# Kernel optimization log

Hardware: AMD Instinct MI355X
Metric: run time of the kernel (lower is better)

## Reference

```python
import jax, jax.numpy as jnp
import numpy as np

NUM_HEADS = 16
H_SELF = 10  # hardcoded h in forward: first 10 heads self-attend, rest cross-attend
DIM = 1024
HEAD_DIM = DIM // NUM_HEADS
SCALE = HEAD_DIM ** -0.5


def _qkv(x, Wqkv):
    # x: [B, N, C] -> q, k, v each [B, H, N, hd]
    B, N, C = x.shape
    qkv = (x @ Wqkv).reshape(B, N, 3, NUM_HEADS, C // NUM_HEADS).transpose(2, 0, 3, 1, 4)
    return qkv[0], qkv[1], qkv[2]


def _attn(q, k, v):
    # q,k,v: [B, h, N, d]
    scores = jnp.einsum('bhqd,bhkd->bhqk', q, k) * SCALE
    probs = jax.nn.softmax(scores, axis=-1)  # attn_drop_ratio = 0.0
    return jnp.einsum('bhqk,bhkd->bhqd', probs, v)


def _proj(xa, xb, Wproj, bproj):
    # xa: [B, 10, N, d], xb: [B, 6, N, d] -> [B, N, C]
    B = xa.shape[0]
    N = xa.shape[2]
    x = jnp.concatenate([xa, xb], axis=1).transpose(0, 2, 1, 3).reshape(B, N, DIM)
    return x @ Wproj + bproj  # proj_drop_ratio = 0.0


def setup_inputs() -> dict:
    key = jax.random.key(0)
    k0, k1, k2, k3 = jax.random.split(key, 4)
    B, N, C = 16, 577, DIM
    x1 = jax.random.normal(k0, (B, N, C), dtype=jnp.float32)
    x2 = jax.random.normal(k1, (B, N, C), dtype=jnp.float32)
    # nn.Linear(dim, dim*3, bias=False): store as [C, 3C] so y = x @ W
    Wqkv = jax.random.normal(k2, (C, 3 * C), dtype=jnp.float32) * 0.02
    # nn.Linear(dim, dim) has bias by default
    Wproj = jax.random.normal(k3, (C, C), dtype=jnp.float32) * 0.02
    bproj = jnp.zeros((C,), dtype=jnp.float32)
    return {"x1": x1, "x2": x2, "Wqkv": Wqkv, "Wproj": Wproj, "bproj": bproj}


def reference(x1, x2, Wqkv, Wproj, bproj):
    q1, k1, v1 = _qkv(x1, Wqkv)
    q2, k2, v2 = _qkv(x2, Wqkv)
    h = H_SELF
    x11 = _attn(q1[:, :h], k1[:, :h], v1[:, :h])  # self-attn branch of x1
    x12 = _attn(q1[:, h:], k2[:, h:], v2[:, h:])  # cross: q from x1, kv from x2
    x22 = _attn(q2[:, :h], k2[:, :h], v2[:, :h])  # self-attn branch of x2
    x21 = _attn(q2[:, h:], k1[:, h:], v1[:, h:])  # cross: q from x2, kv from x1
    out1 = _proj(x11, x12, Wproj, bproj)
    out2 = _proj(x22, x21, Wproj, bproj)
    return (out1, out2)
```

## Files before the change

kernel.cpp:

```cpp
#include <hip/hip_runtime.h>
#include <hip/hip_bf16.h>
#include <stdint.h>
#include <math.h>

typedef __attribute__((ext_vector_type(8))) short bf16x8;
typedef __attribute__((ext_vector_type(4))) float f32x4;
typedef __attribute__((ext_vector_type(8))) unsigned short ushort8;
typedef __attribute__((ext_vector_type(4))) unsigned int uint4v;
typedef __attribute__((ext_vector_type(2))) unsigned int uint2v;

#define NTOK   9232
#define MROWS  18464
#define MPAD   18688
#define NPADV  640
#define QSCALE 0.18033688011112042f

__device__ __forceinline__ uint16_t f2b(float f) {
  uint32_t u = __builtin_bit_cast(uint32_t, f);
  u += 0x7fffu + ((u >> 16) & 1u);
  return (uint16_t)(u >> 16);
}

__device__ __forceinline__ uint32_t packbf(float lo, float hi) {
  return (uint32_t)f2b(lo) | ((uint32_t)f2b(hi) << 16);
}

__device__ __forceinline__ f32x4 mfma16(bf16x8 a, bf16x8 b, f32x4 c) {
  return __builtin_amdgcn_mfma_f32_16x16x32_bf16(a, b, c, 0, 0, 0);
}

__device__ __forceinline__ void gl_lds16(const void* g, void* l) {
  __builtin_amdgcn_global_load_lds(
      (const __attribute__((address_space(1))) uint32_t*)g,
      (__attribute__((address_space(3))) uint32_t*)l, 16, 0, 0);
}

__global__ void convert_x_kernel(const float* __restrict__ x1,
                                 const float* __restrict__ x2,
                                 uint16_t* __restrict__ Xb) {
  const size_t stride = (size_t)gridDim.x * blockDim.x;
  const size_t total8 = (size_t)MPAD * 1024 / 8;
  for (size_t i = (size_t)blockIdx.x * blockDim.x + threadIdx.x; i < total8; i += stride) {
    const size_t e = i * 8;
    const size_t row = e >> 10;
    ushort8 ov;
    if (row < (size_t)MROWS) {
      const float* src = (row < (size_t)NTOK) ? (x1 + e) : (x2 + (e - (size_t)NTOK * 1024));
      float4 a = *(const float4*)(src);
      float4 b = *(const float4*)(src + 4);
      ov[0] = f2b(a.x); ov[1] = f2b(a.y); ov[2] = f2b(a.z); ov[3] = f2b(a.w);
      ov[4] = f2b(b.x); ov[5] = f2b(b.y); ov[6] = f2b(b.z); ov[7] = f2b(b.w);
    } else {
      ov = (ushort8)0;
    }
    *(ushort8*)(Xb + e) = ov;
  }
}

__global__ void transw_kernel(const float* __restrict__ in, uint16_t* __restrict__ out,
                              int R, int Cc) {
  __shared__ float t[32][33];
  const int r0 = blockIdx.x * 32, c0 = blockIdx.y * 32;
  const int tr = threadIdx.x >> 5, tc = threadIdx.x & 31;
#pragma unroll
  for (int i = 0; i < 4; ++i)
    t[tr + i * 8][tc] = in[(size_t)(r0 + tr + i * 8) * Cc + c0 + tc];
  __syncthreads();
#pragma unroll
  for (int i = 0; i < 4; ++i) {
    const int orow = c0 + tr + i * 8;
    out[(size_t)orow * R + r0 + tc] = f2b(t[tc][tr + i * 8]);
  }
}

__global__ void zero_vpad_kernel(uint16_t* __restrict__ Vtb) {
  const int idx = blockIdx.x * 256 + threadIdx.x;
  for (int i = idx; i < 32768 * 8; i += 256 * 256) {
    const int p = i >> 3;
    const int ch = i & 7;
    *(ushort8*)(Vtb + (size_t)p * NPADV + 576 + ch * 8) = (ushort8)0;
  }
}

#define G256_SETUP                                                             \
  const int srow = tt >> 2;                                        \
  const int schunk = tt & 3;                         \
  const int swc = schunk ^ ((srow >> 1) & 3);                                  \
  const int crs = (c >> 1) & 3;                                                \
  char* aL = (char*)As3;                                                       \
  char* bL = (char*)Bs3;                                                       \
  auto SA = [&](int buf, int t) {                                              \
    _Pragma("unroll")                                                          \
    for (int i = 0; i < 2; ++i) {                                              \
      const int row = i * 128 + srow;                                          \
      gl_lds16(aG + (size_t)row * 2048 + t * 64 + (swc << 4),                  \
               aL + buf * 16384 + row * 64 + (schunk << 4));                   \
    }                                                                          \
  };                                                                           \
  auto SB = [&](int buf, int t) {                                              \
    _Pragma("unroll")                                                          \
    for (int i = 0; i < 2; ++i) {                                              \
      const int row = i * 128 + srow;                                          \
      gl_lds16(bG + (size_t)row * 2048 + t * 64 + (swc << 4),                  \
               bL + buf * 16384 + row * 64 + (schunk << 4));                   \
    }                                                                          \
  };                                                                           \
  auto LDA = [&](int buf, int mi) -> bf16x8 {                                  \
    const int r = wm * 128 + mi * 16 + c;                                      \
    return *(const bf16x8*)(aL + buf * 16384 + r * 64 + ((g ^ crs) << 4));     \
  };                                                                           \
  auto LDB = [&](int buf, int ni) -> bf16x8 {                                  \
    const int r = wn * 64 + ni * 16 + c;                                       \
    return *(const bf16x8*)(bL + buf * 16384 + r * 64 + ((g ^ crs) << 4));     \
  };

#define G256_MFMA_BLOCK(BR)                                                    \
  {                                                                            \
    bf16x8 b0 = LDB(BR, 0), b1 = LDB(BR, 1);                                   \
    bf16x8 b2 = LDB(BR, 2), b3 = LDB(BR, 3);                                   \
    __builtin_amdgcn_s_setprio(1);                                             \
    _Pragma("unroll")                                                          \
    for (int mi = 0; mi < 8; ++mi) {                                           \
      const bf16x8 a0 = LDA(BR, mi);                                           \
      acc[mi][0] = mfma16(a0, b0, acc[mi][0]);                                 \
      acc[mi][1] = mfma16(a0, b1, acc[mi][1]);                                 \
      acc[mi][2] = mfma16(a0, b2, acc[mi][2]);                                 \
      acc[mi][3] = mfma16(a0, b3, acc[mi][3]);                                 \
    }                                                                          \
    __builtin_amdgcn_s_setprio(0);                                             \
  }

#define G256R2_ITER(T, BR)                                                     \
  {                                                                            \
    asm volatile("s_waitcnt vmcnt(0)" ::: "memory");                           \
    __builtin_amdgcn_s_barrier();                                              \
    __builtin_amdgcn_sched_barrier(0);                                         \
    if ((T) < 31) { SA((BR) ^ 1, (T) + 1); SB((BR) ^ 1, (T) + 1); }            \
    G256_MFMA_BLOCK(BR)                                                        \
  }

#define G256_KLOOP                                                             \
  G256_SETUP                                                                   \
  SA(0, 0); SB(0, 0);                                                          \
  for (int j2 = 0; j2 < 16; ++j2) {                                            \
    G256R2_ITER(2 * j2, 0)                                                     \
    G256R2_ITER(2 * j2 + 1, 1)                                                 \
  }

__global__ __launch_bounds__(512, 1) void gemm_qkv_kernel(
    const uint16_t* __restrict__ A, const uint16_t* __restrict__ Bt,
    uint16_t* __restrict__ Qb, uint16_t* __restrict__ Kb, uint16_t* __restrict__ Vtb) {
  __shared__ __align__(128) char smem[65536];
  uint16_t* As3 = (uint16_t*)smem;
  uint16_t* Bs3 = (uint16_t*)(smem + 32768);
  const int tt = threadIdx.x;
  const int w = tt >> 6, l = tt & 63;
  const int c = l & 15, g = l >> 4;
  const int wm = w >> 2, wn = w & 3;
  const int orig = blockIdx.x;
  const int xcd = orig & 7, sub8 = orig >> 3;
  const int work = (xcd < 4 ? xcd * 110 : 440 + (xcd - 4) * 109) + sub8;
  int bm, bn;
  {
    const int stripe = work / 36;
    if (stripe >= 24) { bm = 72; bn = work - 864; }
    else {
      const int r2 = work % 36;
      const int bg = r2 / 12, r3 = r2 % 12;
      bm = stripe * 3 + r3 % 3;
      bn = bg * 4 + r3 / 3;
    }
  }
  f32x4 acc[8][4] = {};
  const char* aG = (const char*)(A + (size_t)bm * 256 * 1024);
  const char* bG = (const char*)(Bt + (size_t)bn * 256 * 1024);

  G256_KLOOP

  const int sArea = bn >> 2;
  __syncthreads();
  if (sArea <= 1) {
    uint16_t* outb = (sArea == 0) ? Qb : Kb;
    const float scale = (sArea == 0) ? QSCALE : 1.0f;
#pragma unroll
    for (int q = 0; q < 4; ++q) {
      if (wm == (q >> 1)) {
        char* wbase = smem + (g * 4) * 544 + (wn * 64 + c) * 2;
#pragma unroll
        for (int mi2 = 0; mi2 < 4; ++mi2) {
          const int mi = (q & 1) * 4 + mi2;
#pragma unroll
          for (int r = 0; r < 4; ++r)
#pragma unroll
            for (int ni = 0; ni < 4; ++ni)
              *(uint16_t*)(wbase + mi2 * 8704 + r * 544 + ni * 32) =
                  f2b(acc[mi][ni][r] * scale);
        }
      }
      __syncthreads();
      {
        const int row = tt >> 3, hp = tt & 7;
        const int R = bm * 256 + q * 64 + row;
        if (R < MROWS) {
          const int src = (R >= NTOK) ? 1 : 0;
          const int rr = R - src * NTOK;
          const int bb = rr / 577;
          const int nn = rr - bb * 577;
          const size_t base0 =
              ((((size_t)src * 16 + bb) * 16 + (bn & 3) * 4) * 577 + nn) * 64;
          const char* rbase = smem + row * 544;
#pragma unroll
          for (int j = 0; j < 4; ++j) {
            const int ch = hp + j * 8;
            const int hh2 = ch >> 3;
            const int dd = (ch & 7) * 8;
            const uint4v v = *(const uint4v*)(rbase + ch * 16);
            *(uint4v*)(outb + base0 + (size_t)hh2 * 577 * 64 + dd) = v;
          }
        }
      }
      __syncthreads();
    }
  } else {
#pragma unroll
    for (int half = 0; half < 2; ++half) {
#pragma unroll
      for (int hv = 0; hv < 2; ++hv) {
        if (wm == half && (wn >> 1) == hv) {
          char* wbase = smem + ((wn & 1) * 64 + c) * 272 + g * 8;
#pragma unroll
          for (int mi = 0; mi < 8; ++mi)
#pragma unroll
            for (int ni = 0; ni < 4; ++ni) {
              const uint2v pw = {packbf(acc[mi][ni][0], acc[mi][ni][1]),
                                 packbf(acc[mi][ni][2], acc[mi][ni][3])};
              *(uint2v*)(wbase + ni * 4352 + mi * 32) = pw;
            }
        }
        __syncthreads();
        {
          const int col = tt >> 2, s = tt & 3;
          const int C = bn * 256 + hv * 128 + col;
          const int hh2 = (C >> 6) & 15;
          const int dd = C & 63;
          const char* rbase = smem + col * 272 + s * 64;
#pragma unroll
          for (int j = 0; j < 4; ++j) {
            const int R0 = bm * 256 + half * 128 + s * 32 + j * 8;
            if (R0 >= MROWS) continue;
            const int src0 = (R0 >= NTOK) ? 1 : 0;
            const int rr0 = R0 - src0 * NTOK;
            const int bb0 = rr0 / 577;
            const int nn0 = rr0 - bb0 * 577;
            const uint4v v = *(const uint4v*)(rbase + j * 16);
            const uint16_t* pv = (const uint16_t*)&v;
            const bool fast = (R0 + 7 < MROWS) && (nn0 + 8 <= 577) &&
                              (((R0 + 7) >= NTOK ? 1 : 0) == src0);
            if (fast) {
              uint16_t* dst =
                  Vtb + ((((size_t)src0 * 16 + bb0) * 16 + hh2) * 64 + dd) * NPADV + nn0;
#pragma unroll
              for (int e = 0; e < 8; ++e) dst[e] = pv[e];
            } else {
#pragma unroll
              for (int e = 0; e < 8; ++e) {
                const int R = R0 + e;
                if (R >= MROWS) break;
                const int sx = (R >= NTOK) ? 1 : 0;
                const int rr = R - sx * NTOK;
                const int b2 = rr / 577;
                const int n2 = rr - b2 * 577;
                Vtb[((((size_t)sx * 16 + b2) * 16 + hh2) * 64 + dd) * NPADV + n2] = pv[e];
              }
            }
          }
        }
        __syncthreads();
      }
    }
  }
}

#define GEMM_TRI_SETUP                                                         \
  const int srow4 = tt >> 2;                                        \
  const int schunk = tt & 3;                         \
  const int swc = schunk ^ ((srow4 >> 1) & 3);                                 \
  const int crs = (c >> 1) & 3;                                                \
  char* aL = (char*)As3;                                                       \
  char* bL = (char*)Bs3;                                                       \
  auto SA = [&](int buf, int t) {                                              \
    _Pragma("unroll")                                                          \
    for (int i = 0; i < 2; ++i) {                                              \
      const int row = i * 64 + srow4;                                          \
      gl_lds16(aG + (size_t)row * 2048 + t * 64 + (swc << 4),                  \
               aL + buf * 8192 + row * 64 + (schunk << 4));                    \
    }                                                                          \
  };                                                                           \
  auto SB = [&](int buf, int t) {                                              \
    _Pragma("unroll")                                                          \
    for (int i = 0; i < 2; ++i) {                                              \
      const int row = i * 64 + srow4;                                          \
      gl_lds16(bG + (size_t)row * 2048 + t * 64 + (swc << 4),                  \
               bL + buf * 8192 + row * 64 + (schunk << 4));                    \
    }                                                                          \
  };                                                                           \
  auto LDA = [&](int buf, int mi) -> bf16x8 {                                  \
    const int r = wm * 64 + mi * 16 + c;                                       \
    return *(const bf16x8*)(aL + buf * 8192 + r * 64 + ((g ^ crs) << 4));      \
  };                                                                           \
  auto LDB = [&](int buf, int ni) -> bf16x8 {                                  \
    const int r = wn * 64 + ni * 16 + c;                                       \
    return *(const bf16x8*)(bL + buf * 8192 + r * 64 + ((g ^ crs) << 4));      \
  };

#define G_MFMA_BLOCK(BR)                                                       \
  {                                                                            \
    bf16x8 b0 = LDB(BR, 0), b1 = LDB(BR, 1);                                   \
    bf16x8 b2 = LDB(BR, 2), b3 = LDB(BR, 3);                                   \
    __builtin_amdgcn_s_setprio(1);                                             \
    _Pragma("unroll")                                                          \
    for (int mi = 0; mi < 4; ++mi) {                                           \
      const bf16x8 a0 = LDA(BR, mi);                                           \
      acc[mi][0] = mfma16(a0, b0, acc[mi][0]);                                 \
      acc[mi][1] = mfma16(a0, b1, acc[mi][1]);                                 \
      acc[mi][2] = mfma16(a0, b2, acc[mi][2]);                                 \
      acc[mi][3] = mfma16(a0, b3, acc[mi][3]);                                 \
    }                                                                          \
    __builtin_amdgcn_s_setprio(0);                                             \
  }

#define G_ITER_S(T, BR, BS)                                                    \
  {                                                                            \
    asm volatile("s_waitcnt vmcnt(4)" ::: "memory");                           \
    __builtin_amdgcn_s_barrier();                                              \
    __builtin_amdgcn_sched_barrier(0);                                         \
    SA(BS, (T) + 2); SB(BS, (T) + 2);                                          \
    G_MFMA_BLOCK(BR)                                                           \
  }

#define G_ITER_N(BR, VM)                                                       \
  {                                                                            \
    asm volatile("s_waitcnt vmcnt(" #VM ")" ::: "memory");                     \
    __builtin_amdgcn_s_barrier();                                              \
    __builtin_amdgcn_sched_barrier(0);                                         \
    G_MFMA_BLOCK(BR)                                                           \
  }

#define GEMM_TRI_KLOOP                                                         \
  GEMM_TRI_SETUP                                                               \
  SA(0, 0); SB(0, 0); SA(1, 1); SB(1, 1);                                      \
  for (int j = 0; j < 10; ++j) {                                               \
    const int t3 = j * 3;                                                      \
    G_ITER_S(t3, 0, 2)                                                         \
    G_ITER_S(t3 + 1, 1, 0)                                                     \
    G_ITER_S(t3 + 2, 2, 1)                                                     \
  }                                                                            \
  G_ITER_N(0, 4)                                                               \
  G_ITER_N(1, 0)

#define KVB 64
#define ATT_NT 10
__global__ __launch_bounds__(256, 2) void attn_kernel(
    const uint16_t* __restrict__ Qb, const uint16_t* __restrict__ Kb,
    const uint16_t* __restrict__ Vtb, uint16_t* __restrict__ O) {
  __shared__ __align__(128) char smem[73728];
  const int tid = threadIdx.x;
  const int w = tid >> 6, l = tid & 63;
  const int c = l & 15, g = l >> 4;
  const int bid = blockIdx.x;
  const int qc = bid & 1;
  const int p = bid >> 1;
  const int h = p & 15, b = (p >> 4) & 15, o = p >> 8;
  const int kvsrc = (h < 10) ? o : (1 - o);
  const uint16_t* qp = Qb + (((size_t)o * 16 + b) * 16 + h) * 577 * 64;
  const uint16_t* kp = Kb + (((size_t)kvsrc * 16 + b) * 16 + h) * 577 * 64;
  const uint16_t* vp = Vtb + (((size_t)kvsrc * 16 + b) * 16 + h) * 64 * NPADV;

  const int qbase = qc * 320 + w * 80;

  const int sub = l >> 3;
  const int colEl = (((l & 7) ^ sub) << 3);
  char* KsA = smem;
  char* VsA = smem + 16384;
  char* Pb  = smem + 32768 + w * 10240;
  const int rs = (c & 7) << 4;

  bf16x8 Qf[5][2];
#pragma unroll
  for (int qt = 0; qt < 5; ++qt) {
    const int qrow = min(qbase + qt * 16 + c, 576);
    const uint16_t* qr = qp + (size_t)qrow * 64 + g * 8;
    Qf[qt][0] = *(const bf16x8*)(qr);
    Qf[qt][1] = *(const bf16x8*)(qr + 32);
  }

  f32x4 acc[4][5] = {};
  float m_run[5] = {-3.0e38f, -3.0e38f, -3.0e38f, -3.0e38f, -3.0e38f};
  float l_run[5] = {0.f, 0.f, 0.f, 0.f, 0.f};

  auto STAGE = [&](int buf, int kv0) {
#pragma unroll
    for (int i = 0; i < 2; ++i) {
      const int j = w * 2 + i;
      const int row = j * 8 + sub;
      const int gk = min(kv0 + row, 576);
      gl_lds16(kp + (size_t)gk * 64 + colEl, KsA + buf * 8192 + j * 1024 + l * 16);
      gl_lds16(vp + (size_t)row * NPADV + kv0 + colEl, VsA + buf * 8192 + j * 1024 + l * 16);
    }
  };

  STAGE(0, 0);
  __syncthreads();

  for (int t = 0; t < ATT_NT; ++t) {
    if (t < ATT_NT - 1) STAGE((t + 1) & 1, (t + 1) * KVB);
    {
      const char* Kt = KsA + (t & 1) * 8192;
      const char* Vt = VsA + (t & 1) * 8192;
      bf16x8 Kf[4][2];
#pragma unroll
      for (int kt = 0; kt < 4; ++kt) {
        const char* kr = Kt + (kt * 16 + c) * 128;
        Kf[kt][0] = *(const bf16x8*)(kr + ((g * 16) ^ rs));
        Kf[kt][1] = *(const bf16x8*)(kr + ((64 + g * 16) ^ rs));
      }
      float alpha_[5];
#pragma unroll
      for (int qt = 0; qt < 5; ++qt) {
        f32x4 s[4];
#pragma unroll
        for (int kt = 0; kt < 4; ++kt) {
          f32x4 z = {0.f, 0.f, 0.f, 0.f};
          z = mfma16(Kf[kt][0], Qf[qt][0], z);
          z = mfma16(Kf[kt][1], Qf[qt][1], z);
          s[kt] = z;
        }
        if (t == ATT_NT - 1) {
#pragma unroll
          for (int kt = 0; kt < 4; ++kt)
#pragma unroll
            for (int r = 0; r < 4; ++r) {
              if (kt == 0 && r == 0) { if (g > 0) s[kt][r] = -3.0e38f; }
              else s[kt][r] = -3.0e38f;
            }
        }
        float mt = s[0][0];
#pragma unroll
        for (int kt = 0; kt < 4; ++kt)
#pragma unroll
          for (int r = 0; r < 4; ++r) mt = fmaxf(mt, s[kt][r]);
        mt = fmaxf(mt, __shfl_xor(mt, 16));
        mt = fmaxf(mt, __shfl_xor(mt, 32));
        float al;
        if (mt > m_run[qt] + 8.0f) {
          al = exp2f(m_run[qt] - mt);
          m_run[qt] = mt;
        } else {
          al = 1.0f;
        }
        alpha_[qt] = al;
        const float mcur = m_run[qt];
        float lt = 0.f;
#pragma unroll
        for (int kt = 0; kt < 4; ++kt)
#pragma unroll
          for (int r = 0; r < 4; ++r) {
            const float pv = exp2f(s[kt][r] - mcur);
            s[kt][r] = pv;
            lt += pv;
          }
        lt += __shfl_xor(lt, 16);
        lt += __shfl_xor(lt, 32);
        l_run[qt] = l_run[qt] * al + lt;
        const int rowOff = (qt * 16 + c) * 128;
#pragma unroll
        for (int kt = 0; kt < 4; ++kt) {
          const uint2v pw = {packbf(s[kt][0], s[kt][1]), packbf(s[kt][2], s[kt][3])};
          *(uint2v*)(Pb + rowOff + ((kt * 32 + g * 8) ^ rs)) = pw;
        }
      }
#pragma unroll
      for (int qt = 0; qt < 5; ++qt) {
        if (alpha_[qt] != 1.0f) {
#pragma unroll
          for (int dt = 0; dt < 4; ++dt)
#pragma unroll
            for (int r = 0; r < 4; ++r) acc[dt][qt][r] *= alpha_[qt];
        }
      }
      bf16x8 pf[5][2];
#pragma unroll
      for (int qt = 0; qt < 5; ++qt) {
        const char* pr = Pb + (qt * 16 + c) * 128;
        pf[qt][0] = *(const bf16x8*)(pr + ((g * 16) ^ rs));
        pf[qt][1] = *(const bf16x8*)(pr + ((64 + g * 16) ^ rs));
      }
#pragma unroll
      for (int dt = 0; dt < 4; ++dt) {
        const char* vr = Vt + (dt * 16 + c) * 128;
        const bf16x8 v0 = *(const bf16x8*)(vr + ((g * 16) ^ rs));
        const bf16x8 v1 = *(const bf16x8*)(vr + ((64 + g * 16) ^ rs));
#pragma unroll
        for (int qt = 0; qt < 5; ++qt) {
          acc[dt][qt] = mfma16(v0, pf[qt][0], acc[dt][qt]);
          acc[dt][qt] = mfma16(v1, pf[qt][1], acc[dt][qt]);
        }
      }
    }
    __syncthreads();
  }

  {
#pragma unroll
    for (int qt = 0; qt < 5; ++qt) {
      const float inv = 1.0f / l_run[qt];
      const int rowOff = (qt * 16 + c) * 128;
#pragma unroll
      for (int dt = 0; dt < 4; ++dt) {
        const uint2v pw = {packbf(acc[dt][qt][0] * inv, acc[dt][qt][1] * inv),
                           packbf(acc[dt][qt][2] * inv, acc[dt][qt][3] * inv)};
        *(uint2v*)(Pb + rowOff + ((dt * 32 + g * 8) ^ rs)) = pw;
      }
    }
    const size_t obase = ((size_t)o * NTOK + (size_t)b * 577) * 1024 + h * 64;
#pragma unroll
    for (int pass = 0; pass < 10; ++pass) {
      const int row = pass * 8 + (l >> 3);
      const int tok = qbase + row;
      const uint4v vv = *(const uint4v*)(Pb + row * 128 + (((l & 7) * 16) ^ ((row & 7) << 4)));
      if (tok <= 576)
        *(uint4v*)(O + obase + (size_t)tok * 1024 + (l & 7) * 8) = vv;
    }
  }
}

__global__ __launch_bounds__(256, 3) void gemm_proj_kernel(
    const uint16_t* __restrict__ A, const uint16_t* __restrict__ Bt,
    const float* __restrict__ bias, float* __restrict__ out) {
  __shared__ uint16_t As3[3][4096];
  __shared__ uint16_t Bs3[3][4096];
  const int tt = threadIdx.x;
  const int w = tt >> 6, l = tt & 63;
  const int c = l & 15, g = l >> 4;
  const int wgid = blockIdx.x;
  const int work = (wgid & 7) * 145 + (wgid >> 3);
  int bm, bn;
  {
    const int stripe = work / 48;
    if (stripe >= 24) { bm = 144; bn = work - 24 * 48; }
    else { const int r3 = work % 48; bm = stripe * 6 + r3 % 6; bn = r3 / 6; }
  }
  const int wm = w >> 1, wn = w & 1;
  f32x4 acc[4][4] = {};
  const char* aG = (const char*)(A + (size_t)bm * 128 * 1024);
  const char* bG = (const char*)(Bt + (size_t)bn * 128 * 1024);

  GEMM_TRI_KLOOP

#pragma unroll
  for (int mi = 0; mi < 4; ++mi) {
#pragma unroll
    for (int r = 0; r < 4; ++r) {
      const int R = bm * 128 + wm * 64 + mi * 16 + g * 4 + r;
      if (R >= MROWS) continue;
#pragma unroll
      for (int ni = 0; ni < 4; ++ni) {
        const int C = bn * 128 + wn * 64 + ni * 16 + c;
        out[(size_t)R * 1024 + C] = acc[mi][ni][r] + bias[C];
      }
    }
  }
}

extern "C" void kernel_launch(void* const* d_in, const int* in_sizes, int n_in,
                              void* d_out, int out_size, void* d_ws, size_t ws_size,
                              hipStream_t stream) {
  (void)in_sizes; (void)n_in; (void)out_size; (void)ws_size;
  const float* x1    = (const float*)d_in[0];
  const float* x2    = (const float*)d_in[1];
  const float* Wqkv  = (const float*)d_in[2];
  const float* Wproj = (const float*)d_in[3];
  const float* bproj = (const float*)d_in[4];
  float* out = (float*)d_out;

  char* ws = (char*)d_ws;
  size_t off = 0;
  auto alloc = [&](size_t bytes) -> char* {
    char* p = ws + off;
    off += (bytes + 255) & ~(size_t)255;
    return p;
  };
  uint16_t* Xb     = (uint16_t*)alloc((size_t)MPAD * 1024 * 2);
  uint16_t* Wqkvt  = (uint16_t*)alloc((size_t)3072 * 1024 * 2);
  uint16_t* Wprojt = (uint16_t*)alloc((size_t)1024 * 1024 * 2);
  uint16_t* Qb     = (uint16_t*)alloc((size_t)512 * 577 * 64 * 2);
  uint16_t* Kb     = (uint16_t*)alloc((size_t)512 * 577 * 64 * 2);
  uint16_t* Vtb    = (uint16_t*)alloc((size_t)512 * 64 * NPADV * 2);

  zero_vpad_kernel<<<256, 256, 0, stream>>>(Vtb);
  convert_x_kernel<<<2048, 256, 0, stream>>>(x1, x2, Xb);
  transw_kernel<<<dim3(32, 96), 256, 0, stream>>>(Wqkv, Wqkvt, 1024, 3072);
  transw_kernel<<<dim3(32, 32), 256, 0, stream>>>(Wproj, Wprojt, 1024, 1024);
  gemm_qkv_kernel<<<876, 512, 0, stream>>>(Xb, Wqkvt, Qb, Kb, Vtb);
  attn_kernel<<<1024, 256, 0, stream>>>(Qb, Kb, Vtb, Xb );
  gemm_proj_kernel<<<1160, 256, 0, stream>>>(Xb, Wprojt, bproj, out);
}
```

Before: 347.9 us.

## Retile projection GEMM to 256x256 blocks and prioritize attention MFMAs

```diff
diff --git a/kernel.cpp b/kernel.cpp
--- a/kernel.cpp
+++ b/kernel.cpp
@@ -281,82 +281,45 @@
   }
 }
 
-#define GEMM_TRI_SETUP                                                         \
-  const int srow4 = tt >> 2;                                        \
-  const int schunk = tt & 3;                         \
-  const int swc = schunk ^ ((srow4 >> 1) & 3);                                 \
-  const int crs = (c >> 1) & 3;                                                \
-  char* aL = (char*)As3;                                                       \
-  char* bL = (char*)Bs3;                                                       \
-  auto SA = [&](int buf, int t) {                                              \
-    _Pragma("unroll")                                                          \
-    for (int i = 0; i < 2; ++i) {                                              \
-      const int row = i * 64 + srow4;                                          \
-      gl_lds16(aG + (size_t)row * 2048 + t * 64 + (swc << 4),                  \
-               aL + buf * 8192 + row * 64 + (schunk << 4));                    \
-    }                                                                          \
-  };                                                                           \
-  auto SB = [&](int buf, int t) {                                              \
-    _Pragma("unroll")                                                          \
-    for (int i = 0; i < 2; ++i) {                                              \
-      const int row = i * 64 + srow4;                                          \
-      gl_lds16(bG + (size_t)row * 2048 + t * 64 + (swc << 4),                  \
-               bL + buf * 8192 + row * 64 + (schunk << 4));                    \
-    }                                                                          \
-  };                                                                           \
-  auto LDA = [&](int buf, int mi) -> bf16x8 {                                  \
-    const int r = wm * 64 + mi * 16 + c;                                       \
-    return *(const bf16x8*)(aL + buf * 8192 + r * 64 + ((g ^ crs) << 4));      \
-  };                                                                           \
-  auto LDB = [&](int buf, int ni) -> bf16x8 {                                  \
-    const int r = wn * 64 + ni * 16 + c;                                       \
-    return *(const bf16x8*)(bL + buf * 8192 + r * 64 + ((g ^ crs) << 4));      \
-  };
-
-#define G_MFMA_BLOCK(BR)                                                       \
-  {                                                                            \
-    bf16x8 b0 = LDB(BR, 0), b1 = LDB(BR, 1);                                   \
-    bf16x8 b2 = LDB(BR, 2), b3 = LDB(BR, 3);                                   \
-    __builtin_amdgcn_s_setprio(1);                                             \
-    _Pragma("unroll")                                                          \
-    for (int mi = 0; mi < 4; ++mi) {                                           \
-      const bf16x8 a0 = LDA(BR, mi);                                           \
-      acc[mi][0] = mfma16(a0, b0, acc[mi][0]);                                 \
-      acc[mi][1] = mfma16(a0, b1, acc[mi][1]);                                 \
-      acc[mi][2] = mfma16(a0, b2, acc[mi][2]);                                 \
-      acc[mi][3] = mfma16(a0, b3, acc[mi][3]);                                 \
-    }                                                                          \
-    __builtin_amdgcn_s_setprio(0);                                             \
-  }
-
-#define G_ITER_S(T, BR, BS)                                                    \
-  {                                                                            \
-    asm volatile("s_waitcnt vmcnt(4)" ::: "memory");                           \
-    __builtin_amdgcn_s_barrier();                                              \
-    __builtin_amdgcn_sched_barrier(0);                                         \
-    SA(BS, (T) + 2); SB(BS, (T) + 2);                                          \
-    G_MFMA_BLOCK(BR)                                                           \
-  }
-
-#define G_ITER_N(BR, VM)                                                       \
-  {                                                                            \
-    asm volatile("s_waitcnt vmcnt(" #VM ")" ::: "memory");                     \
-    __builtin_amdgcn_s_barrier();                                              \
-    __builtin_amdgcn_sched_barrier(0);                                         \
-    G_MFMA_BLOCK(BR)                                                           \
-  }
-
-#define GEMM_TRI_KLOOP                                                         \
-  GEMM_TRI_SETUP                                                               \
-  SA(0, 0); SB(0, 0); SA(1, 1); SB(1, 1);                                      \
-  for (int j = 0; j < 10; ++j) {                                               \
-    const int t3 = j * 3;                                                      \
-    G_ITER_S(t3, 0, 2)                                                         \
-    G_ITER_S(t3 + 1, 1, 0)                                                     \
-    G_ITER_S(t3 + 2, 2, 1)                                                     \
-  }                                                                            \
-  G_ITER_N(0, 4)                                                               \
-  G_ITER_N(1, 0)
+__global__ __launch_bounds__(512, 1) void gemm_proj_kernel(
+    const uint16_t* __restrict__ A, const uint16_t* __restrict__ Bt,
+    const float* __restrict__ bias, float* __restrict__ out) {
+  __shared__ __align__(128) char smem[65536];
+  uint16_t* As3 = (uint16_t*)smem;
+  uint16_t* Bs3 = (uint16_t*)(smem + 32768);
+  const int tt = threadIdx.x;
+  const int w = tt >> 6, l = tt & 63;
+  const int c = l & 15, g = l >> 4;
+  const int wm = w >> 2, wn = w & 3;
+  const int orig = blockIdx.x;
+  const int xcd = orig & 7, sub8 = orig >> 3;
+  const int work = (xcd < 4 ? xcd * 37 : 148 + (xcd - 4) * 36) + sub8;
+  int bm, bn;
+  {
+    const int stripe = work / 12;
+    if (stripe >= 24) { bm = 72; bn = work - 288; }
+    else { const int r3 = work % 12; bm = stripe * 3 + r3 % 3; bn = r3 / 3; }
+  }
+  f32x4 acc[8][4] = {};
+  const char* aG = (const char*)(A + (size_t)bm * 256 * 1024);
+  const char* bG = (const char*)(Bt + (size_t)bn * 256 * 1024);
+
+  G256_KLOOP
+
+#pragma unroll
+  for (int mi = 0; mi < 8; ++mi) {
+#pragma unroll
+    for (int r = 0; r < 4; ++r) {
+      const int R = bm * 256 + wm * 128 + mi * 16 + g * 4 + r;
+      if (R >= MROWS) continue;
+#pragma unroll
+      for (int ni = 0; ni < 4; ++ni) {
+        const int C = bn * 256 + wn * 64 + ni * 16 + c;
+        out[(size_t)R * 1024 + C] = acc[mi][ni][r] + bias[C];
+      }
+    }
+  }
+}
 
 #define KVB 64
 #define ATT_NT 10
@@ -428,6 +391,7 @@
 #pragma unroll
       for (int qt = 0; qt < 5; ++qt) {
         f32x4 s[4];
+        __builtin_amdgcn_s_setprio(1);
 #pragma unroll
         for (int kt = 0; kt < 4; ++kt) {
           f32x4 z = {0.f, 0.f, 0.f, 0.f};
@@ -435,6 +399,7 @@
           z = mfma16(Kf[kt][1], Qf[qt][1], z);
           s[kt] = z;
         }
+        __builtin_amdgcn_s_setprio(0);
         if (t == ATT_NT - 1) {
 #pragma unroll
           for (int kt = 0; kt < 4; ++kt)
@@ -495,6 +460,7 @@
         pf[qt][0] = *(const bf16x8*)(pr + ((g * 16) ^ rs));
         pf[qt][1] = *(const bf16x8*)(pr + ((64 + g * 16) ^ rs));
       }
+      __builtin_amdgcn_s_setprio(1);
 #pragma unroll
       for (int dt = 0; dt < 4; ++dt) {
         const char* vr = Vt + (dt * 16 + c) * 128;
@@ -506,6 +472,7 @@
           acc[dt][qt] = mfma16(v1, pf[qt][1], acc[dt][qt]);
         }
       }
+      __builtin_amdgcn_s_setprio(0);
     }
     __syncthreads();
   }
@@ -530,44 +497,6 @@
       const uint4v vv = *(const uint4v*)(Pb + row * 128 + (((l & 7) * 16) ^ ((row & 7) << 4)));
       if (tok <= 576)
         *(uint4v*)(O + obase + (size_t)tok * 1024 + (l & 7) * 8) = vv;
-    }
-  }
-}
-
-__global__ __launch_bounds__(256, 3) void gemm_proj_kernel(
-    const uint16_t* __restrict__ A, const uint16_t* __restrict__ Bt,
-    const float* __restrict__ bias, float* __restrict__ out) {
-  __shared__ uint16_t As3[3][4096];
-  __shared__ uint16_t Bs3[3][4096];
-  const int tt = threadIdx.x;
-  const int w = tt >> 6, l = tt & 63;
-  const int c = l & 15, g = l >> 4;
-  const int wgid = blockIdx.x;
-  const int work = (wgid & 7) * 145 + (wgid >> 3);
-  int bm, bn;
-  {
-    const int stripe = work / 48;
-    if (stripe >= 24) { bm = 144; bn = work - 24 * 48; }
-    else { const int r3 = work % 48; bm = stripe * 6 + r3 % 6; bn = r3 / 6; }
-  }
-  const int wm = w >> 1, wn = w & 1;
-  f32x4 acc[4][4] = {};
-  const char* aG = (const char*)(A + (size_t)bm * 128 * 1024);
-  const char* bG = (const char*)(Bt + (size_t)bn * 128 * 1024);
-
-  GEMM_TRI_KLOOP
-
-#pragma unroll
-  for (int mi = 0; mi < 4; ++mi) {
-#pragma unroll
-    for (int r = 0; r < 4; ++r) {
-      const int R = bm * 128 + wm * 64 + mi * 16 + g * 4 + r;
-      if (R >= MROWS) continue;
-#pragma unroll
-      for (int ni = 0; ni < 4; ++ni) {
-        const int C = bn * 128 + wn * 64 + ni * 16 + c;
-        out[(size_t)R * 1024 + C] = acc[mi][ni][r] + bias[C];
-      }
     }
   }
 }
@@ -603,5 +532,5 @@
   transw_kernel<<<dim3(32, 32), 256, 0, stream>>>(Wproj, Wprojt, 1024, 1024);
   gemm_qkv_kernel<<<876, 512, 0, stream>>>(Xb, Wqkvt, Qb, Kb, Vtb);
   attn_kernel<<<1024, 256, 0, stream>>>(Qb, Kb, Vtb, Xb );
-  gemm_proj_kernel<<<1160, 256, 0, stream>>>(Xb, Wprojt, bproj, out);
-}
+  gemm_proj_kernel<<<292, 512, 0, stream>>>(Xb, Wprojt, bproj, out);
+}
```

Result: slower. 361.5 us (+3.9%).
